# Optimization experiments

Measured on AMD Instinct MI355X. Metric: run time of the kernel, lower is better.

Reference implementation:

```python
import jax, jax.numpy as jnp
import numpy as np

NUM_VIEWS = 8
GAMMA = 10.0
EPS = 1e-06
B, LMAX, D = 16, 4096, 1024


def setup_inputs() -> dict:
    key = jax.random.key(0)
    k1, k2, k3 = jax.random.split(key, 3)
    v_pad = jax.random.normal(k1, (B, LMAX, D), dtype=jnp.float32)
    centers = jax.random.uniform(k2, (B, NUM_VIEWS, 2), dtype=jnp.float32)
    # per-sample grid sizes: H, W in [32, 64) so L = H*W <= LMAX (64*64 padding)
    hw = jax.random.randint(k3, (B, 2), 32, 64, dtype=jnp.int32)
    grid_thws = jnp.concatenate([jnp.ones((B, 1), jnp.int32), hw], axis=1)  # [B, 3] = (t, H, W)
    v_len = (hw[:, 0] * hw[:, 1]).astype(jnp.int32)
    return {"v_pad": v_pad, "centers": centers, "v_len": v_len, "grid_thws": grid_thws}


def reference(v_pad, centers, v_len, grid_thws):
    # v_pad: [B, Lmax, D]; centers: [B, V, 2]; grid_thws: [B, 3] ints (t, H, W)
    Lmax = v_pad.shape[1]
    H = grid_thws[:, 1]  # [B]
    W = grid_thws[:, 2]  # [B]
    l = jnp.arange(Lmax, dtype=jnp.int32)  # [L] row-major index into the HxW grid
    i = l[None, :] // W[:, None]           # [B, L] grid row
    j = l[None, :] % W[:, None]            # [B, L] grid col
    y = (i.astype(v_pad.dtype) + 0.5) / H[:, None].astype(v_pad.dtype)
    x = (j.astype(v_pad.dtype) + 0.5) / W[:, None].astype(v_pad.dtype)
    valid = (l[None, :] < (H * W)[:, None])  # [B, L] mask padded rows
    coords = jnp.stack([x, y], axis=-1)      # [B, L, 2] (x, y) as in torch code
    diff = centers[:, :, None, :] - coords[:, None, :, :]   # [B, V, L, 2]
    dist_sq = jnp.sum(diff * diff, axis=-1)                 # [B, V, L]
    m = jnp.exp(-GAMMA * dist_sq) * valid[:, None, :].astype(v_pad.dtype)
    numerator = jnp.einsum('bvl,bld->bvd', m, v_pad)        # [B, V, D]
    denominator = jnp.sum(m, axis=-1, keepdims=True) + EPS  # [B, V, 1]
    return numerator / denominator
```

## Files before the change

kernel.cpp:

```cpp
#include <hip/hip_runtime.h>

#define NV 8
#define NB 16
#define LMAX 4096
#define ND 1024
#define CHUNK 128
#define NCHUNK (LMAX / CHUNK)
#define EPS_ 1e-6f
#define NEXP10 (-14.426950408889634f)

#define PNUM_FLOATS ((size_t)NB * NCHUNK * NV * ND)

__global__ __launch_bounds__(256, 4) void dvs_accum(
    const float* __restrict__ v_pad,
    const float* __restrict__ centers,
    const int* __restrict__ grid_thws,
    float* __restrict__ pnum,
    float* __restrict__ pden)
{
    const int bid   = blockIdx.x;
    const int b     = bid >> 5;
    const int chunk = bid & (NCHUNK - 1);
    const int H  = grid_thws[b * 3 + 1];
    const int W  = grid_thws[b * 3 + 2];
    const int HW = H * W;
    const int l0 = chunk * CHUNK;
    if (l0 >= HW) return;
    const int rr = (min(CHUNK, HW - l0) + 3) & ~3;

    __shared__ __align__(16) float wlds[CHUNK][NV];

    const int t = threadIdx.x;

    const float4* __restrict__ src =
        (const float4*)v_pad + ((size_t)b * LMAX + l0) * (ND / 4) + t;
    float4 c0 = src[0 * 256];
    float4 c1 = src[1 * 256];
    float4 c2 = src[2 * 256];
    float4 c3 = src[3 * 256];

    const float invH = 1.0f / (float)H;
    const float invW = 1.0f / (float)W;
#pragma unroll
    for (int g = 0; g < 4; ++g) {
        const int idx = t + g * 256;
        const int row = idx >> 3;
        const int v   = idx & 7;
        const int l   = l0 + row;
        const int i   = l / W;
        const int j   = l - i * W;
        const float y = ((float)i + 0.5f) * invH;
        const float x = ((float)j + 0.5f) * invW;
        const float2 c = ((const float2*)centers)[b * NV + v];
        const float dx = c.x - x;
        const float dy = c.y - y;
        const float s  = fmaf(dy, dy, dx * dx);
        wlds[row][v] = (l < HW) ? exp2f(s * NEXP10) : 0.0f;
    }
    __syncthreads();

    const size_t pbase = (size_t)(b * NCHUNK + chunk) * NV;
    if (t < 64) {
        const int rg = t >> 3;
        const int v  = t & 7;
        float s = 0.0f;
#pragma unroll
        for (int k = 0; k < CHUNK / 8; ++k) s += wlds[rg + 8 * k][v];
        s += __shfl_xor(s, 8);
        s += __shfl_xor(s, 16);
        s += __shfl_xor(s, 32);
        if (rg == 0) pden[pbase + v] = s;
    }

    float acc[NV][4];
#pragma unroll
    for (int v = 0; v < NV; ++v)
#pragma unroll
        for (int k = 0; k < 4; ++k) acc[v][k] = 0.0f;

    auto proc = [&](const int r, const float4 r4) {
        float w[NV];
        *(float4*)&w[0] = *(const float4*)&wlds[r][0];
        *(float4*)&w[4] = *(const float4*)&wlds[r][4];
#pragma unroll
        for (int v = 0; v < NV; ++v) {
            acc[v][0] = fmaf(w[v], r4.x, acc[v][0]);
            acc[v][1] = fmaf(w[v], r4.y, acc[v][1]);
            acc[v][2] = fmaf(w[v], r4.z, acc[v][2]);
            acc[v][3] = fmaf(w[v], r4.w, acc[v][3]);
        }
    };

    for (int r = 0; r < rr; r += 4) {
        float4 n0 = c0, n1 = c1, n2 = c2, n3 = c3;
        if (r + 4 < rr) {
            n0 = src[(r + 4) * 256];
            n1 = src[(r + 5) * 256];
            n2 = src[(r + 6) * 256];
            n3 = src[(r + 7) * 256];
        }
        proc(r + 0, c0); proc(r + 1, c1); proc(r + 2, c2); proc(r + 3, c3);
        c0 = n0; c1 = n1; c2 = n2; c3 = n3;
    }

    float4* np_ = (float4*)pnum;
#pragma unroll
    for (int v = 0; v < NV; ++v)
        np_[(pbase + v) * (ND / 4) + t] =
            make_float4(acc[v][0], acc[v][1], acc[v][2], acc[v][3]);
}

__global__ __launch_bounds__(64) void dvs_reduce(
    const float* __restrict__ pnum,
    const float* __restrict__ pden,
    const int* __restrict__ grid_thws,
    float* __restrict__ out)
{
    const int bv = blockIdx.x >> 2;
    const int q  = blockIdx.x & 3;
    const int b  = bv >> 3;
    const int v  = bv & (NV - 1);
    const int HW = grid_thws[b * 3 + 1] * grid_thws[b * 3 + 2];
    const int nc = (HW + CHUNK - 1) / CHUNK;
    const int t  = threadIdx.x;
    const int f4 = q * 64 + t;

    const float4* np_ = (const float4*)pnum;
    const size_t cstride = (size_t)NV * (ND / 4);
    const size_t base = ((size_t)b * NCHUNK * NV + v) * (ND / 4) + f4;
    const int dbase = b * NCHUNK * NV + v;

    float4 s0 = make_float4(0.f, 0.f, 0.f, 0.f), s1 = s0, s2 = s0, s3 = s0;
    float d0 = 0.f, d1 = 0.f, d2 = 0.f, d3 = 0.f;
    int c = 0;
    for (; c + 4 <= nc; c += 4) {
        float4 p0 = np_[base + (size_t)(c + 0) * cstride];
        float4 p1 = np_[base + (size_t)(c + 1) * cstride];
        float4 p2 = np_[base + (size_t)(c + 2) * cstride];
        float4 p3 = np_[base + (size_t)(c + 3) * cstride];
        d0 += pden[dbase + (c + 0) * NV];
        d1 += pden[dbase + (c + 1) * NV];
        d2 += pden[dbase + (c + 2) * NV];
        d3 += pden[dbase + (c + 3) * NV];
        s0.x += p0.x; s0.y += p0.y; s0.z += p0.z; s0.w += p0.w;
        s1.x += p1.x; s1.y += p1.y; s1.z += p1.z; s1.w += p1.w;
        s2.x += p2.x; s2.y += p2.y; s2.z += p2.z; s2.w += p2.w;
        s3.x += p3.x; s3.y += p3.y; s3.z += p3.z; s3.w += p3.w;
    }
    for (; c < nc; ++c) {
        float4 p0 = np_[base + (size_t)c * cstride];
        d0 += pden[dbase + c * NV];
        s0.x += p0.x; s0.y += p0.y; s0.z += p0.z; s0.w += p0.w;
    }
    const float inv = 1.0f / (d0 + d1 + d2 + d3 + EPS_);
    float4 o = make_float4((s0.x + s1.x + s2.x + s3.x) * inv,
                           (s0.y + s1.y + s2.y + s3.y) * inv,
                           (s0.z + s1.z + s2.z + s3.z) * inv,
                           (s0.w + s1.w + s2.w + s3.w) * inv);
    ((float4*)out)[(size_t)bv * (ND / 4) + f4] = o;
}

extern "C" void kernel_launch(void* const* d_in, const int* in_sizes, int n_in,
                              void* d_out, int out_size, void* d_ws, size_t ws_size,
                              hipStream_t stream) {
    const float* v_pad     = (const float*)d_in[0];
    const float* centers   = (const float*)d_in[1];
    const int*   grid_thws = (const int*)d_in[3];

    float* pnum = (float*)d_ws;
    float* pden = pnum + PNUM_FLOATS;

    dvs_accum<<<NB * NCHUNK, 256, 0, stream>>>(v_pad, centers, grid_thws, pnum, pden);
    dvs_reduce<<<NB * NV * 4, 64, 0, stream>>>(pnum, pden, grid_thws, (float*)d_out);
}
```

Before: 33.24 us.

## Fuse cross-chunk reduction into accumulation kernel via last-block atomic counter

Merges the separate reduce kernel into the accumulation kernel. Each block bumps a per-batch atomic counter after writing its partials, and the last-arriving block sums all chunk partials and normalizes the output. This removes a kernel launch and its gap, but puts the whole reduction for a batch on one block running serially after the others, and adds a memset launch to clear the counters.

```diff
diff --git a/kernel.cpp b/kernel.cpp
--- a/kernel.cpp
+++ b/kernel.cpp
@@ -10,13 +10,16 @@
 #define NEXP10 (-14.426950408889634f)
 
 #define PNUM_FLOATS ((size_t)NB * NCHUNK * NV * ND)
+#define PDEN_FLOATS ((size_t)NB * NCHUNK * NV)
 
-__global__ __launch_bounds__(256, 4) void dvs_accum(
+__global__ __launch_bounds__(256, 4) void dvs_fused(
     const float* __restrict__ v_pad,
     const float* __restrict__ centers,
     const int* __restrict__ grid_thws,
     float* __restrict__ pnum,
-    float* __restrict__ pden)
+    float* __restrict__ pden,
+    int* __restrict__ counters,
+    float* __restrict__ out)
 {
     const int bid   = blockIdx.x;
     const int b     = bid >> 5;
@@ -24,11 +27,14 @@
     const int H  = grid_thws[b * 3 + 1];
     const int W  = grid_thws[b * 3 + 2];
     const int HW = H * W;
+    const int nc = (HW + CHUNK - 1) / CHUNK;
     const int l0 = chunk * CHUNK;
     if (l0 >= HW) return;
     const int rr = (min(CHUNK, HW - l0) + 3) & ~3;
 
     __shared__ __align__(16) float wlds[CHUNK][NV];
+    __shared__ int amLast;
+    __shared__ float dls[NV];
 
     const int t = threadIdx.x;
 
@@ -108,56 +114,41 @@
     for (int v = 0; v < NV; ++v)
         np_[(pbase + v) * (ND / 4) + t] =
             make_float4(acc[v][0], acc[v][1], acc[v][2], acc[v][3]);
-}
 
-__global__ __launch_bounds__(64) void dvs_reduce(
-    const float* __restrict__ pnum,
-    const float* __restrict__ pden,
-    const int* __restrict__ grid_thws,
-    float* __restrict__ out)
-{
-    const int bv = blockIdx.x >> 2;
-    const int q  = blockIdx.x & 3;
-    const int b  = bv >> 3;
-    const int v  = bv & (NV - 1);
-    const int HW = grid_thws[b * 3 + 1] * grid_thws[b * 3 + 2];
-    const int nc = (HW + CHUNK - 1) / CHUNK;
-    const int t  = threadIdx.x;
-    const int f4 = q * 64 + t;
+    __threadfence();
+    if (t == 0)
+        amLast = (atomicAdd(&counters[b], 1) == nc - 1);
+    __syncthreads();
+    if (!amLast) return;
+    __threadfence();
 
-    const float4* np_ = (const float4*)pnum;
-    const size_t cstride = (size_t)NV * (ND / 4);
-    const size_t base = ((size_t)b * NCHUNK * NV + v) * (ND / 4) + f4;
-    const int dbase = b * NCHUNK * NV + v;
+    if (t < NV) {
+        float s = 0.0f;
+        for (int c = 0; c < nc; ++c)
+            s += pden[(size_t)(b * NCHUNK + c) * NV + t];
+        dls[t] = s;
+    }
+    __syncthreads();
 
-    float4 s0 = make_float4(0.f, 0.f, 0.f, 0.f), s1 = s0, s2 = s0, s3 = s0;
-    float d0 = 0.f, d1 = 0.f, d2 = 0.f, d3 = 0.f;
-    int c = 0;
-    for (; c + 4 <= nc; c += 4) {
-        float4 p0 = np_[base + (size_t)(c + 0) * cstride];
-        float4 p1 = np_[base + (size_t)(c + 1) * cstride];
-        float4 p2 = np_[base + (size_t)(c + 2) * cstride];
-        float4 p3 = np_[base + (size_t)(c + 3) * cstride];
-        d0 += pden[dbase + (c + 0) * NV];
-        d1 += pden[dbase + (c + 1) * NV];
-        d2 += pden[dbase + (c + 2) * NV];
-        d3 += pden[dbase + (c + 3) * NV];
-        s0.x += p0.x; s0.y += p0.y; s0.z += p0.z; s0.w += p0.w;
-        s1.x += p1.x; s1.y += p1.y; s1.z += p1.z; s1.w += p1.w;
-        s2.x += p2.x; s2.y += p2.y; s2.z += p2.z; s2.w += p2.w;
-        s3.x += p3.x; s3.y += p3.y; s3.z += p3.z; s3.w += p3.w;
+    float4 r8[NV];
+#pragma unroll
+    for (int v = 0; v < NV; ++v) r8[v] = make_float4(0.f, 0.f, 0.f, 0.f);
+    const float4* rp = (const float4*)pnum;
+    for (int c = 0; c < nc; ++c) {
+        const size_t cb = (size_t)(b * NCHUNK + c) * NV * (ND / 4) + t;
+#pragma unroll
+        for (int v = 0; v < NV; ++v) {
+            float4 p = rp[cb + (size_t)v * (ND / 4)];
+            r8[v].x += p.x; r8[v].y += p.y; r8[v].z += p.z; r8[v].w += p.w;
+        }
     }
-    for (; c < nc; ++c) {
-        float4 p0 = np_[base + (size_t)c * cstride];
-        d0 += pden[dbase + c * NV];
-        s0.x += p0.x; s0.y += p0.y; s0.z += p0.z; s0.w += p0.w;
+    float4* o4 = (float4*)out + (size_t)b * NV * (ND / 4) + t;
+#pragma unroll
+    for (int v = 0; v < NV; ++v) {
+        const float inv = 1.0f / (dls[v] + EPS_);
+        o4[(size_t)v * (ND / 4)] = make_float4(r8[v].x * inv, r8[v].y * inv,
+                                               r8[v].z * inv, r8[v].w * inv);
     }
-    const float inv = 1.0f / (d0 + d1 + d2 + d3 + EPS_);
-    float4 o = make_float4((s0.x + s1.x + s2.x + s3.x) * inv,
-                           (s0.y + s1.y + s2.y + s3.y) * inv,
-                           (s0.z + s1.z + s2.z + s3.z) * inv,
-                           (s0.w + s1.w + s2.w + s3.w) * inv);
-    ((float4*)out)[(size_t)bv * (ND / 4) + f4] = o;
 }
 
 extern "C" void kernel_launch(void* const* d_in, const int* in_sizes, int n_in,
@@ -167,9 +158,11 @@
     const float* centers   = (const float*)d_in[1];
     const int*   grid_thws = (const int*)d_in[3];
 
-    float* pnum = (float*)d_ws;
-    float* pden = pnum + PNUM_FLOATS;
+    float* pnum     = (float*)d_ws;
+    float* pden     = pnum + PNUM_FLOATS;
+    int*   counters = (int*)(pden + PDEN_FLOATS);
 
-    dvs_accum<<<NB * NCHUNK, 256, 0, stream>>>(v_pad, centers, grid_thws, pnum, pden);
-    dvs_reduce<<<NB * NV * 4, 64, 0, stream>>>(pnum, pden, grid_thws, (float*)d_out);
+    hipMemsetAsync(counters, 0, NB * sizeof(int), stream);
+    dvs_fused<<<NB * NCHUNK, 256, 0, stream>>>(v_pad, centers, grid_thws,
+                                               pnum, pden, counters, (float*)d_out);
 }
```

Result: slower. 92.94 us (+179.6%).
